# Performance work log

Hardware: AMD Instinct MI355X
Metric: run time of the kernel (lower is better)

## Reference

```python
import jax, jax.numpy as jnp
import numpy as np

B, V, C, A = 32, 48, 24, 6
NC, D, H, OUT = 10000, 128, 128, 167


def setup_inputs() -> dict:
    key = jax.random.key(0)
    ks = jax.random.split(key, 12)
    seqs = jax.random.randint(ks[0], (B, V, C), 0, NC + 1)
    ancestors = jax.random.randint(ks[1], (B, V, C, A), 0, NC + 1)
    length = jax.random.randint(ks[2], (B,), 1, V + 1)
    amask = (jax.random.uniform(ks[3], (B, V, C, A)) < 0.7).astype(jnp.float32)
    amask = amask.at[..., 0].set(1.0)  # first ancestor always valid
    emb = jax.random.normal(ks[4], (NC + 1, D), dtype=jnp.float32) * 0.02
    emb = emb.at[NC].set(0.0)  # padding row is zeros
    w_basic = jax.random.normal(ks[5], (D, 2 * D), dtype=jnp.float32) * (1.0 / np.sqrt(2 * D))
    u_basic_w = jax.random.normal(ks[6], (1, D), dtype=jnp.float32) * (1.0 / np.sqrt(D))
    u_basic_b = jnp.zeros((1,), jnp.float32)
    gru_wih = jax.random.normal(ks[7], (3 * H, D), dtype=jnp.float32) * (1.0 / np.sqrt(H))
    gru_whh = jax.random.normal(ks[8], (3 * H, H), dtype=jnp.float32) * (1.0 / np.sqrt(H))
    gru_bih = jnp.zeros((3 * H,), jnp.float32)
    gru_bhh = jnp.zeros((3 * H,), jnp.float32)
    out_w = jax.random.normal(ks[9], (OUT, H), dtype=jnp.float32) * (1.0 / np.sqrt(H))
    out_b = jnp.zeros((OUT,), jnp.float32)
    return dict(seqs=seqs, ancestors=ancestors, length=length, ancestor_length=amask,
                emb=emb, w_basic=w_basic, u_basic_w=u_basic_w, u_basic_b=u_basic_b,
                gru_wih=gru_wih, gru_whh=gru_whh, gru_bih=gru_bih, gru_bhh=gru_bhh,
                out_w=out_w, out_b=out_b)


def _gram_forward(seqs, ancestors, length, ancestor_length, emb, w_basic,
                  u_basic_w, u_basic_b, gru_wih, gru_whh, gru_bih, gru_bhh,
                  out_w, out_b):
    # gather embeddings
    seqs_e = emb[seqs]            # [B,V,C,D]
    anc_e = emb[ancestors]        # [B,V,C,A,D]
    seqs_rep = jnp.broadcast_to(seqs_e[..., None, :], anc_e.shape)
    # Bahdanau attention: mask applied to concat BEFORE the linear (as in source)
    cat = jnp.concatenate([seqs_rep, anc_e], axis=-1) * ancestor_length[..., None]  # [B,V,C,A,2D]
    hdd = jnp.tanh(jnp.einsum('bvcad,ed->bvcae', cat, w_basic))  # [B,V,C,A,D]
    score = jnp.einsum('bvcad,od->bvcao', hdd, u_basic_w) + u_basic_b  # [B,V,C,A,1]
    # mask_softmax over ancestor axis, faithful to the source (sum==0 -> -1)
    e = jnp.exp(score) * ancestor_length[..., None]
    s = jnp.sum(e, axis=3, keepdims=True)
    s = jnp.where(s == 0, -1.0, s)
    attn = e / s                  # [B,V,C,A,1]
    ctx = jnp.sum(attn * anc_e, axis=3)            # [B,V,C,D] weighted ancestor sum
    x = jnp.tanh(jnp.sum(ctx, axis=2))             # [B,V,D] visit embedding

    # single-layer GRU over visits (valid steps form a prefix, padded tail masked below)
    hsz = gru_whh.shape[1]
    def step(hstate, xt):
        gi = xt @ gru_wih.T + gru_bih              # [B,3H]
        gh = hstate @ gru_whh.T + gru_bhh
        ir, iz, inn = jnp.split(gi, 3, axis=-1)
        hr, hz, hn = jnp.split(gh, 3, axis=-1)
        r = jax.nn.sigmoid(ir + hr)
        z = jax.nn.sigmoid(iz + hz)
        n = jnp.tanh(inn + r * hn)
        hnew = (1.0 - z) * n + z * hstate
        return hnew, hnew
    h0 = jnp.zeros((x.shape[0], hsz), x.dtype)
    _, outs = jax.lax.scan(step, h0, jnp.swapaxes(x, 0, 1))  # [V,B,H]
    outs = jnp.swapaxes(outs, 0, 1)                          # [B,V,H]

    visit_mask = (jnp.arange(x.shape[1])[None, :] < length[:, None]).astype(x.dtype)
    context = jnp.einsum('bv,bvh->bh', visit_mask, outs)     # masked sum over visits
    logit = jax.nn.sigmoid(context @ out_w.T + out_b)        # dropout=eval (identity)
    return logit


def reference(seqs, ancestors, length, ancestor_length, emb, w_basic, u_basic_w,
              u_basic_b, gru_wih, gru_whh, gru_bih, gru_bhh, out_w, out_b):
    return _gram_forward(seqs, ancestors, length, ancestor_length, emb, w_basic,
                         u_basic_w, u_basic_b, gru_wih, gru_whh, gru_bih, gru_bhh,
                         out_w, out_b)
```

## Files before the change

kernel.cpp:

```cpp
#include <hip/hip_runtime.h>

#define BB 32
#define VV 48
#define CC 24
#define AA 6
#define NCODES 10001
#define DD 128
#define HH 128
#define OUTN 167
#define G3 384

__device__ __forceinline__ float fast_tanh(float x) {
    return 1.0f - 2.0f / (1.0f + __expf(2.0f * x));
}
__device__ __forceinline__ float fast_sigmoid(float x) {
    return 1.0f / (1.0f + __expf(-x));
}

__global__ __launch_bounds__(256) void k_precompute(
    const float* __restrict__ emb, const float* __restrict__ w_basic,
    float* __restrict__ P1, float* __restrict__ P2, int nrows)
{
    __shared__ float embs[8][128];
    int row0 = blockIdx.x * 8;
    int t = threadIdx.x;
    for (int i = t; i < 8 * 128; i += 256) {
        int r = i >> 7, d = i & 127;
        int row = row0 + r;
        embs[r][d] = (row < nrows) ? emb[row * 128 + d] : 0.0f;
    }
    __syncthreads();
    int e = t & 127, sel = t >> 7;
    const float* wrow = w_basic + e * 256 + sel * 128;
    float acc[8] = {0, 0, 0, 0, 0, 0, 0, 0};
#pragma unroll 8
    for (int d = 0; d < 128; ++d) {
        float w = wrow[d];
#pragma unroll
        for (int r = 0; r < 8; ++r) acc[r] += embs[r][d] * w;
    }
    float* dst = sel ? P2 : P1;
#pragma unroll
    for (int r = 0; r < 8; ++r) {
        int row = row0 + r;
        if (row < nrows) dst[row * 128 + e] = acc[r];
    }
}

__global__ __launch_bounds__(256) void k_attention(
    const int* __restrict__ seqs, const int* __restrict__ ancestors,
    const float* __restrict__ amask, const float* __restrict__ emb,
    const float* __restrict__ P1, const float* __restrict__ P2,
    const float* __restrict__ u_w, const float* __restrict__ u_b,
    float* __restrict__ x_out)
{
    __shared__ float u_s[128];
    __shared__ float sc_s[144];
    __shared__ float m_s[144];
    __shared__ int   anc_s[144];
    __shared__ float attn_s[144];
    __shared__ float sum_s[24];
    __shared__ float xred[256];
    int bv = blockIdx.x;
    int t = threadIdx.x;
    if (t < 128) u_s[t] = u_w[t];
    __syncthreads();
    float ub = u_b[0];
    int g = t >> 2, l = t & 3;
    for (int p = g; p < CC * AA; p += 64) {
        int c = p / AA, a = p - c * AA;
        int sidx = bv * CC + c;
        int s_code = seqs[sidx];
        int aidx = sidx * AA + a;
        int anc = ancestors[aidx];
        float m = amask[aidx];
        const float* p1 = P1 + s_code * 128;
        const float* p2 = P2 + anc * 128;
        float partial = 0.0f;
        int e0 = l * 32;
#pragma unroll 8
        for (int j = 0; j < 32; ++j) {
            int e = e0 + j;
            float hv = fast_tanh(m * (p1[e] + p2[e]));
            partial += hv * u_s[e];
        }
        partial += __shfl_xor(partial, 1);
        partial += __shfl_xor(partial, 2);
        if (l == 0) {
            sc_s[p] = partial + ub;
            m_s[p] = m;
            anc_s[p] = anc;
        }
    }
    __syncthreads();
    if (t < CC * AA) attn_s[t] = __expf(sc_s[t]) * m_s[t];
    __syncthreads();
    if (t < CC) {
        float s = 0.0f;
#pragma unroll
        for (int a = 0; a < AA; ++a) s += attn_s[t * AA + a];
        sum_s[t] = (s == 0.0f) ? -1.0f : s;
    }
    __syncthreads();
    if (t < CC * AA) attn_s[t] = attn_s[t] / sum_s[t / AA];
    __syncthreads();
    int e = t & 127, hc = t >> 7;
    float acc = 0.0f;
    for (int c = hc * 12; c < hc * 12 + 12; ++c) {
#pragma unroll
        for (int a = 0; a < AA; ++a) {
            int p = c * AA + a;
            acc += attn_s[p] * emb[anc_s[p] * 128 + e];
        }
    }
    xred[t] = acc;
    __syncthreads();
    if (t < 128) {
        x_out[bv * 128 + t] = fast_tanh(xred[t] + xred[t + 128]);
    }
}

__global__ __launch_bounds__(384) void k_gi(
    const float* __restrict__ x, const float* __restrict__ wih,
    const float* __restrict__ bih, float* __restrict__ gi)
{
    __shared__ float xs[8][128];
    int row0 = blockIdx.x * 8;
    int t = threadIdx.x;
    for (int i = t; i < 8 * 128; i += 384) {
        int r = i >> 7, d = i & 127;
        xs[r][d] = x[(row0 + r) * 128 + d];
    }
    __syncthreads();
    const float* wrow = wih + t * 128;
    float acc[8] = {0, 0, 0, 0, 0, 0, 0, 0};
#pragma unroll 8
    for (int d = 0; d < 128; ++d) {
        float w = wrow[d];
#pragma unroll
        for (int r = 0; r < 8; ++r) acc[r] += xs[r][d] * w;
    }
    float bb = bih[t];
#pragma unroll
    for (int r = 0; r < 8; ++r) gi[(row0 + r) * G3 + t] = acc[r] + bb;
}

__global__ __launch_bounds__(768) void k_gru(
    const float* __restrict__ gi, const float* __restrict__ whh,
    const float* __restrict__ bhh, const int* __restrict__ length,
    const float* __restrict__ out_w, const float* __restrict__ out_b,
    float* __restrict__ out)
{
    __shared__ float hs[128];
    __shared__ float part[768];
    __shared__ float bhh_s[384];
    __shared__ float ctxs[128];
    int b = blockIdx.x;
    int t = threadIdx.x;
    int o = t >> 1, half = t & 1;
    float rw[64];
    const float* wsrc = whh + o * 128 + half * 64;
#pragma unroll
    for (int j = 0; j < 64; ++j) rw[j] = wsrc[j];
    if (t < 128) hs[t] = 0.0f;
    if (t < 384) bhh_s[t] = bhh[t];
    int len = length[b];
    float ctx = 0.0f;
    __syncthreads();
    const float* gib = gi + b * VV * G3;
    for (int v = 0; v < VV; ++v) {
        float gir = 0.0f, giz = 0.0f, gin = 0.0f;
        if (t < 128) {
            const float* g = gib + v * G3;
            gir = g[t]; giz = g[128 + t]; gin = g[256 + t];
        }
        float partial = 0.0f;
        const float* hp = hs + half * 64;
#pragma unroll
        for (int j = 0; j < 64; ++j) partial += hp[j] * rw[j];
        part[t] = partial;
        __syncthreads();
        if (t < 128) {
            float gh_r = part[2 * t] + part[2 * t + 1] + bhh_s[t];
            float gh_z = part[2 * (128 + t)] + part[2 * (128 + t) + 1] + bhh_s[128 + t];
            float gh_n = part[2 * (256 + t)] + part[2 * (256 + t) + 1] + bhh_s[256 + t];
            float r = fast_sigmoid(gir + gh_r);
            float z = fast_sigmoid(giz + gh_z);
            float n = fast_tanh(gin + r * gh_n);
            float hnew = (1.0f - z) * n + z * hs[t];
            if (v < len) ctx += hnew;
            hs[t] = hnew;
        }
        __syncthreads();
    }
    if (t < 128) ctxs[t] = ctx;
    __syncthreads();
    if (t < OUTN) {
        const float* wrow = out_w + t * 128;
        float acc = 0.0f;
#pragma unroll 8
        for (int d = 0; d < 128; ++d) acc += ctxs[d] * wrow[d];
        out[b * OUTN + t] = fast_sigmoid(acc + out_b[t]);
    }
}

extern "C" void kernel_launch(void* const* d_in, const int* in_sizes, int n_in,
                              void* d_out, int out_size, void* d_ws, size_t ws_size,
                              hipStream_t stream) {
    const int*   seqs      = (const int*)d_in[0];
    const int*   ancestors = (const int*)d_in[1];
    const int*   length    = (const int*)d_in[2];
    const float* amask     = (const float*)d_in[3];
    const float* emb       = (const float*)d_in[4];
    const float* w_basic   = (const float*)d_in[5];
    const float* u_w       = (const float*)d_in[6];
    const float* u_b       = (const float*)d_in[7];
    const float* wih       = (const float*)d_in[8];
    const float* whh       = (const float*)d_in[9];
    const float* bih       = (const float*)d_in[10];
    const float* bhh       = (const float*)d_in[11];
    const float* out_w     = (const float*)d_in[12];
    const float* out_b     = (const float*)d_in[13];
    float* out = (float*)d_out;

    float* ws = (float*)d_ws;
    float* P1 = ws;
    float* P2 = P1 + NCODES * 128;
    float* x  = P2 + NCODES * 128;
    float* gi = x + BB * VV * 128;

    k_precompute<<<(NCODES + 7) / 8, 256, 0, stream>>>(emb, w_basic, P1, P2, NCODES);
    k_attention<<<BB * VV, 256, 0, stream>>>(seqs, ancestors, amask, emb, P1, P2, u_w, u_b, x);
    k_gi<<<(BB * VV) / 8, 384, 0, stream>>>(x, wih, bih, gi);
    k_gru<<<BB, 768, 0, stream>>>(gi, whh, bhh, length, out_w, out_b, out);
}
```

Measured before the change: 139.3 us.

## Restructure GRU recurrence to one barrier per step and vectorize loads with float4

Rewrites the GRU kernel so each thread pair handles all three gates of one hidden unit, holding 192 weights in registers, combining halves via a lane shuffle and double-buffering the hidden state. This removes the shared partial-sum buffer and one of the two barriers per timestep, and shrinks the block from 768 to 256 threads. The precompute, attention and gi kernels switch to float4 loads and dot products to cut load instruction count. The risk is higher register pressure in the GRU kernel from the larger per-thread weight set.

```diff
diff --git a/kernel.cpp b/kernel.cpp
--- a/kernel.cpp
+++ b/kernel.cpp
@@ -16,28 +16,36 @@
 __device__ __forceinline__ float fast_sigmoid(float x) {
     return 1.0f / (1.0f + __expf(-x));
 }
+__device__ __forceinline__ float dot4(float4 a, float4 b) {
+    return a.x * b.x + a.y * b.y + a.z * b.z + a.w * b.w;
+}
 
 __global__ __launch_bounds__(256) void k_precompute(
     const float* __restrict__ emb, const float* __restrict__ w_basic,
     float* __restrict__ P1, float* __restrict__ P2, int nrows)
 {
-    __shared__ float embs[8][128];
+    __shared__ __align__(16) float embs[8][128];
     int row0 = blockIdx.x * 8;
     int t = threadIdx.x;
-    for (int i = t; i < 8 * 128; i += 256) {
-        int r = i >> 7, d = i & 127;
+    {
+        int r = t >> 5;
         int row = row0 + r;
-        embs[r][d] = (row < nrows) ? emb[row * 128 + d] : 0.0f;
+        float4 v = make_float4(0.f, 0.f, 0.f, 0.f);
+        if (row < nrows) v = ((const float4*)emb)[row * 32 + (t & 31)];
+        ((float4*)embs)[t] = v;
     }
     __syncthreads();
     int e = t & 127, sel = t >> 7;
-    const float* wrow = w_basic + e * 256 + sel * 128;
+    const float4* wrow4 = (const float4*)(w_basic + e * 256 + sel * 128);
     float acc[8] = {0, 0, 0, 0, 0, 0, 0, 0};
-#pragma unroll 8
-    for (int d = 0; d < 128; ++d) {
-        float w = wrow[d];
-#pragma unroll
-        for (int r = 0; r < 8; ++r) acc[r] += embs[r][d] * w;
+#pragma unroll
+    for (int d4 = 0; d4 < 32; ++d4) {
+        float4 wv = wrow4[d4];
+#pragma unroll
+        for (int r = 0; r < 8; ++r) {
+            float4 ev = ((const float4*)embs[r])[d4];
+            acc[r] += dot4(ev, wv);
+        }
     }
     float* dst = sel ? P2 : P1;
 #pragma unroll
@@ -54,7 +62,7 @@
     const float* __restrict__ u_w, const float* __restrict__ u_b,
     float* __restrict__ x_out)
 {
-    __shared__ float u_s[128];
+    __shared__ __align__(16) float u_s[128];
     __shared__ float sc_s[144];
     __shared__ float m_s[144];
     __shared__ int   anc_s[144];
@@ -74,15 +82,20 @@
         int aidx = sidx * AA + a;
         int anc = ancestors[aidx];
         float m = amask[aidx];
-        const float* p1 = P1 + s_code * 128;
-        const float* p2 = P2 + anc * 128;
+        const float4* p14 = (const float4*)(P1 + s_code * 128);
+        const float4* p24 = (const float4*)(P2 + anc * 128);
+        const float4* u4 = (const float4*)u_s;
         float partial = 0.0f;
-        int e0 = l * 32;
-#pragma unroll 8
-        for (int j = 0; j < 32; ++j) {
-            int e = e0 + j;
-            float hv = fast_tanh(m * (p1[e] + p2[e]));
-            partial += hv * u_s[e];
+        int e4 = l * 8;
+#pragma unroll
+        for (int j = 0; j < 8; ++j) {
+            float4 av = p14[e4 + j];
+            float4 bv_ = p24[e4 + j];
+            float4 uv = u4[e4 + j];
+            partial += fast_tanh(m * (av.x + bv_.x)) * uv.x;
+            partial += fast_tanh(m * (av.y + bv_.y)) * uv.y;
+            partial += fast_tanh(m * (av.z + bv_.z)) * uv.z;
+            partial += fast_tanh(m * (av.w + bv_.w)) * uv.w;
         }
         partial += __shfl_xor(partial, 1);
         partial += __shfl_xor(partial, 2);
@@ -124,83 +137,118 @@
     const float* __restrict__ x, const float* __restrict__ wih,
     const float* __restrict__ bih, float* __restrict__ gi)
 {
-    __shared__ float xs[8][128];
+    __shared__ __align__(16) float xs[8][128];
     int row0 = blockIdx.x * 8;
     int t = threadIdx.x;
-    for (int i = t; i < 8 * 128; i += 384) {
-        int r = i >> 7, d = i & 127;
-        xs[r][d] = x[(row0 + r) * 128 + d];
-    }
-    __syncthreads();
-    const float* wrow = wih + t * 128;
+    for (int i = t; i < 8 * 32; i += 384) {
+        ((float4*)xs)[i] = ((const float4*)x)[row0 * 32 + i];
+    }
+    __syncthreads();
+    const float4* wrow4 = (const float4*)(wih + t * 128);
     float acc[8] = {0, 0, 0, 0, 0, 0, 0, 0};
-#pragma unroll 8
-    for (int d = 0; d < 128; ++d) {
-        float w = wrow[d];
-#pragma unroll
-        for (int r = 0; r < 8; ++r) acc[r] += xs[r][d] * w;
+#pragma unroll
+    for (int d4 = 0; d4 < 32; ++d4) {
+        float4 wv = wrow4[d4];
+#pragma unroll
+        for (int r = 0; r < 8; ++r) {
+            float4 xv = ((const float4*)xs[r])[d4];
+            acc[r] += dot4(xv, wv);
+        }
     }
     float bb = bih[t];
 #pragma unroll
     for (int r = 0; r < 8; ++r) gi[(row0 + r) * G3 + t] = acc[r] + bb;
 }
 
-__global__ __launch_bounds__(768) void k_gru(
+__global__ __launch_bounds__(256, 1) void k_gru(
     const float* __restrict__ gi, const float* __restrict__ whh,
     const float* __restrict__ bhh, const int* __restrict__ length,
     const float* __restrict__ out_w, const float* __restrict__ out_b,
     float* __restrict__ out)
 {
-    __shared__ float hs[128];
-    __shared__ float part[768];
-    __shared__ float bhh_s[384];
-    __shared__ float ctxs[128];
+    __shared__ __align__(16) float hs[2][128];
+    __shared__ __align__(16) float ctxs[128];
     int b = blockIdx.x;
     int t = threadIdx.x;
     int o = t >> 1, half = t & 1;
-    float rw[64];
-    const float* wsrc = whh + o * 128 + half * 64;
-#pragma unroll
-    for (int j = 0; j < 64; ++j) rw[j] = wsrc[j];
-    if (t < 128) hs[t] = 0.0f;
-    if (t < 384) bhh_s[t] = bhh[t];
+
+    float4 wr[16], wz[16], wn[16];
+    {
+        const float4* wr4 = (const float4*)(whh + o * 128 + half * 64);
+        const float4* wz4 = (const float4*)(whh + (128 + o) * 128 + half * 64);
+        const float4* wn4 = (const float4*)(whh + (256 + o) * 128 + half * 64);
+#pragma unroll
+        for (int j = 0; j < 16; ++j) {
+            wr[j] = wr4[j];
+            wz[j] = wz4[j];
+            wn[j] = wn4[j];
+        }
+    }
+    float bhr = 0.f, bhz = 0.f, bhn = 0.f;
+    if (half == 0) {
+        bhr = bhh[o];
+        bhz = bhh[128 + o];
+        bhn = bhh[256 + o];
+    }
+    if (t < 128) hs[0][t] = 0.0f;
     int len = length[b];
     float ctx = 0.0f;
     __syncthreads();
+
     const float* gib = gi + b * VV * G3;
+    int cur = 0;
     for (int v = 0; v < VV; ++v) {
-        float gir = 0.0f, giz = 0.0f, gin = 0.0f;
-        if (t < 128) {
+        float gir = 0.f, giz = 0.f, gin = 0.f;
+        if (half == 0) {
             const float* g = gib + v * G3;
-            gir = g[t]; giz = g[128 + t]; gin = g[256 + t];
-        }
-        float partial = 0.0f;
-        const float* hp = hs + half * 64;
-#pragma unroll
-        for (int j = 0; j < 64; ++j) partial += hp[j] * rw[j];
-        part[t] = partial;
+            gir = g[o];
+            giz = g[128 + o];
+            gin = g[256 + o];
+        }
+        const float4* h4 = ((const float4*)hs[cur]) + half * 16;
+        float ar0 = 0.f, ar1 = 0.f, az0 = 0.f, az1 = 0.f, an0 = 0.f, an1 = 0.f;
+#pragma unroll
+        for (int j = 0; j < 16; j += 2) {
+            float4 h0 = h4[j];
+            float4 h1 = h4[j + 1];
+            ar0 += dot4(wr[j], h0);
+            ar1 += dot4(wr[j + 1], h1);
+            az0 += dot4(wz[j], h0);
+            az1 += dot4(wz[j + 1], h1);
+            an0 += dot4(wn[j], h0);
+            an1 += dot4(wn[j + 1], h1);
+        }
+        float ar = ar0 + ar1;
+        float az = az0 + az1;
+        float an = an0 + an1;
+        ar += __shfl_xor(ar, 1);
+        az += __shfl_xor(az, 1);
+        an += __shfl_xor(an, 1);
+        if (half == 0) {
+            float r = fast_sigmoid(gir + ar + bhr);
+            float z = fast_sigmoid(giz + az + bhz);
+            float n = fast_tanh(gin + r * (an + bhn));
+            float hold = hs[cur][o];
+            float hnew = (1.0f - z) * n + z * hold;
+            hs[cur ^ 1][o] = hnew;
+            if (v < len) ctx += hnew;
+        }
+        cur ^= 1;
         __syncthreads();
-        if (t < 128) {
-            float gh_r = part[2 * t] + part[2 * t + 1] + bhh_s[t];
-            float gh_z = part[2 * (128 + t)] + part[2 * (128 + t) + 1] + bhh_s[128 + t];
-            float gh_n = part[2 * (256 + t)] + part[2 * (256 + t) + 1] + bhh_s[256 + t];
-            float r = fast_sigmoid(gir + gh_r);
-            float z = fast_sigmoid(giz + gh_z);
-            float n = fast_tanh(gin + r * gh_n);
-            float hnew = (1.0f - z) * n + z * hs[t];
-            if (v < len) ctx += hnew;
-            hs[t] = hnew;
-        }
-        __syncthreads();
-    }
-    if (t < 128) ctxs[t] = ctx;
+    }
+
+    if (half == 0) ctxs[o] = ctx;
     __syncthreads();
     if (t < OUTN) {
-        const float* wrow = out_w + t * 128;
-        float acc = 0.0f;
-#pragma unroll 8
-        for (int d = 0; d < 128; ++d) acc += ctxs[d] * wrow[d];
-        out[b * OUTN + t] = fast_sigmoid(acc + out_b[t]);
+        const float4* w4 = (const float4*)(out_w + t * 128);
+        const float4* c4 = (const float4*)ctxs;
+        float a0 = 0.f, a1 = 0.f;
+#pragma unroll
+        for (int j = 0; j < 32; j += 2) {
+            a0 += dot4(w4[j], c4[j]);
+            a1 += dot4(w4[j + 1], c4[j + 1]);
+        }
+        out[b * OUTN + t] = fast_sigmoid(a0 + a1 + out_b[t]);
     }
 }
 
@@ -232,5 +280,5 @@
     k_precompute<<<(NCODES + 7) / 8, 256, 0, stream>>>(emb, w_basic, P1, P2, NCODES);
     k_attention<<<BB * VV, 256, 0, stream>>>(seqs, ancestors, amask, emb, P1, P2, u_w, u_b, x);
     k_gi<<<(BB * VV) / 8, 384, 0, stream>>>(x, wih, bih, gi);
-    k_gru<<<BB, 768, 0, stream>>>(gi, whh, bhh, length, out_w, out_b, out);
-}
+    k_gru<<<BB, 256, 0, stream>>>(gi, whh, bhh, length, out_w, out_b, out);
+}
```

New measurement: 406.4 us. +191.7%, slower.
